# Kernel optimization log

Measured on AMD Instinct MI355X. Metric: run time of the kernel, lower is better.

## Reference

```python
import jax, jax.numpy as jnp
from jax import lax
import numpy as np


def setup_inputs() -> dict:
    key = jax.random.key(0)
    ks = jax.random.split(key, 5)
    B = 256
    data = jax.random.normal(ks[0], (B, 1, 28, 28), jnp.float32)
    # ConvLayer: Conv2d(1->256, k=9, s=1)
    w1 = jax.random.normal(ks[1], (256, 1, 9, 9), jnp.float32) * 0.1
    b1 = jnp.zeros((256,), jnp.float32)
    # PrimaryCaps: Conv2d(256->256, k=9, s=2)
    w2 = jax.random.normal(ks[2], (256, 256, 9, 9), jnp.float32) * 0.02
    b2 = jnp.zeros((256,), jnp.float32)
    # DigitCaps routing weights: (in_caps=1152, out_caps=10, out_len=16, in_len=8)
    W = jax.random.normal(ks[3], (1152, 10, 16, 8), jnp.float32) * 0.05
    return {"data": data, "w1": w1, "b1": b1, "w2": w2, "b2": b2, "W": W}


def _squash(s):
    # s: (B,1,10,16); sn*s / ((1+sn)*sqrt(sn)) as in the torch code
    sn = jnp.sum(s * s, axis=-1, keepdims=True)
    return sn * s / ((1.0 + sn) * jnp.sqrt(sn))


def reference(data, w1, b1, w2, b2, W):
    # ConvLayer: conv k9 s1 VALID + relu -> (B,256,20,20)
    x = lax.conv(data, w1, (1, 1), 'VALID') + b1[None, :, None, None]
    x = jax.nn.relu(x)
    # PrimaryCaps: conv k9 s2 VALID -> (B,256,6,6)
    x = lax.conv(x, w2, (2, 2), 'VALID') + b2[None, :, None, None]
    B = x.shape[0]
    # toCapsules: (B,256,6,6) -> (B,8,32,6,6) -> (B,8,1152) -> (B,1152,8)
    x = x.reshape(B, 8, -1).transpose(0, 2, 1)
    # u_hat[b,n,o,k] = W[n,o,k,d] @ x[b,n,d]  -> (B,1152,10,16)
    u_hat = jnp.einsum('nokd,bnd->bnok', W, x)
    b_ij = jnp.zeros((B, 1152, 10, 1), u_hat.dtype)
    num_iterations = 3
    v_j = None
    for it in range(1, num_iterations + 1):
        c_ij = jax.nn.softmax(b_ij, axis=1)            # over input capsules
        s_j = jnp.sum(c_ij * u_hat, axis=1, keepdims=True)  # (B,1,10,16)
        v_j = _squash(s_j)
        if it < num_iterations:
            # Faithful to the torch code: a_ij = u_hat * sum_k(v_j), broadcast
            # over input capsules; b_ij widens to (B,1152,10,16) after iter 1.
            a_ij = u_hat * jnp.sum(v_j, axis=-1, keepdims=True)
            b_ij = b_ij + a_ij
    return v_j[:, 0]  # (B,10,16)
```

## Files before the change

kernel.cpp:

```cpp
#include <hip/hip_runtime.h>
#include <hip/hip_bf16.h>
#include <cmath>


typedef float f32x4 __attribute__((ext_vector_type(4)));
typedef short s16x8 __attribute__((ext_vector_type(8)));
typedef unsigned int u32;

static __device__ __forceinline__ short f2bf(float x) {
  __hip_bfloat16 h = __float2bfloat16(x);
  return *reinterpret_cast<short*>(&h);
}
static __device__ __forceinline__ float bf2f(short s) {
  __hip_bfloat16 h;
  *reinterpret_cast<short*>(&h) = s;
  return __bfloat162float(h);
}
static __device__ __forceinline__ void stage16(const short* g, short* l) {
  __builtin_amdgcn_global_load_lds(
      (const __attribute__((address_space(1))) u32*)(const void*)g,
      (__attribute__((address_space(3))) u32*)(void*)l, 16, 0, 0);
}

#define CHUNK_SHORTS 23552
#define ODD_OFS 12288

__global__ __launch_bounds__(256) void prep_all(
    const float* __restrict__ w2, s16x8* __restrict__ wstg,
    const float* __restrict__ data, const float* __restrict__ w1,
    const float* __restrict__ b1, short* __restrict__ c1g) {
  __shared__ float sbuf[12784];
  const int t = threadIdx.x;
  if (blockIdx.x < 512) {
    const int b = blockIdx.x;
    const int chunk = b >> 6;
    const int kg = (b >> 4) & 3;
    const int cot = b & 15;
    const int co0 = cot * 16;
    const size_t gbase = (size_t)(chunk * 32 + kg * 8) * 81;
    for (int i = t; i < 10368; i += 256) {
      const int r = i / 648, e = i - r * 648;
      sbuf[i] = w2[(size_t)(co0 + r) * 20736 + gbase + e];
    }
    __syncthreads();
    for (int p = t; p < 1296; p += 256) {
      const int tap = p >> 4, co = p & 15;
      s16x8 hi, lo;
#pragma unroll
      for (int i = 0; i < 8; ++i) {
        const float x = sbuf[co * 648 + i * 81 + tap];
        const short h = f2bf(x);
        hi[i] = h;
        lo[i] = f2bf(x - bf2f(h));
      }
      const size_t T = (size_t)(chunk * 81 + tap);
      wstg[T * 2048 + kg * 256 + co0 + co] = hi;
      wstg[T * 2048 + 1024 + kg * 256 + co0 + co] = lo;
    }
    return;
  }
  const int cb = blockIdx.x - 512;
  const int img = cb >> 1;
  const int chh = cb & 1;
  float* simg = sbuf;
  short* c1buf = (short*)&sbuf[1008];
  for (int i = t; i < 784; i += 256)
    simg[(i / 28) * 36 + (i % 28)] = data[img * 784 + i];
  __syncthreads();
  for (int cc = 0; cc < 4; ++cc) {
    const int chunk = chh * 4 + cc;
    for (int task = t; task < 608; task += 256) {
      const int ci = task & 31;
      const int y = task >> 5;
      const int ch = chunk * 32 + ci;
      const float* wr = w1 + ch * 81;
      float acc[20];
      const float bz = b1[ch];
#pragma unroll
      for (int x = 0; x < 20; ++x) acc[x] = bz;
#pragma unroll
      for (int ky = 0; ky < 9; ++ky) {
        float rr[28];
#pragma unroll
        for (int q = 0; q < 7; ++q)
          *(float4*)&rr[q * 4] = *(const float4*)&simg[(y + ky) * 36 + q * 4];
#pragma unroll
        for (int kx = 0; kx < 9; ++kx) {
          const float w = wr[ky * 9 + kx];
#pragma unroll
          for (int x = 0; x < 20; ++x) acc[x] = fmaf(w, rr[x + kx], acc[x]);
        }
      }
      const int kg = ci >> 3, il = ci & 7;
#pragma unroll
      for (int x = 0; x < 19; ++x) {
        const int xh = x >> 1;
        const int r = (x & 1) ? (y * 9 + xh) : (y * 10 + xh);
        short* base = c1buf + ((x & 1) ? ODD_OFS : 0);
        const float v = fmaxf(acc[x], 0.f);
        const short hi = f2bf(v);
        const short lo = f2bf(v - bf2f(hi));
        base[r * 64 + (((kg + r) & 7) << 3) + il] = hi;
        base[r * 64 + (((kg + 4 + r) & 7) << 3) + il] = lo;
      }
    }
    __syncthreads();
    {
      s16x8* dst = (s16x8*)(c1g + (size_t)(img * 8 + chunk) * CHUNK_SHORTS);
      const s16x8* srcb = (const s16x8*)c1buf;
      for (int i = t; i < 2944; i += 256) dst[i] = srcb[i];
    }
    __syncthreads();
  }
}

__global__ __launch_bounds__(256) void conv2_mfma(
    const short* __restrict__ c1g, const short* __restrict__ wstg,
    const float* __restrict__ b2, float* __restrict__ xcaps0,
    float* __restrict__ xcaps1) {
  const int t = threadIdx.x;
  const int bid = blockIdx.x;
  const int xcd = bid & 7;
  const int ksp = xcd & 1;
  const int coh = (xcd >> 1) & 1;
  const int img = (bid >> 3) * 2 + (xcd >> 2);
  const int lane = t & 63;
  const int wv = t >> 6;
  const int r16 = lane & 15;
  const int kg = lane >> 4;

  __shared__ short c1[12288];

  int arowE[3], arowO[3];
#pragma unroll
  for (int m = 0; m < 3; ++m) {
    int pos = m * 16 + r16;
    if (pos > 35) pos = 35;
    const int oy = pos / 6, ox = pos % 6;
    arowE[m] = oy * 20 + ox;
    arowO[m] = oy * 18 + ox;
  }
  int bOff[2], con[2];
  float bias[2];
#pragma unroll
  for (int j = 0; j < 2; ++j) {
    const int co = coh * 128 + wv * 32 + j * 16 + r16;
    con[j] = co;
    bOff[j] = kg * 256 + co;
    bias[j] = (ksp == 0) ? b2[co] : 0.f;
  }
  float* xcp = (ksp == 0) ? xcaps0 : xcaps1;

  const f32x4 vzero = {0.f, 0.f, 0.f, 0.f};
  f32x4 acc[3][2];
#pragma unroll
  for (int m = 0; m < 3; ++m)
#pragma unroll
    for (int j = 0; j < 2; ++j) acc[m][j] = vzero;

  const s16x8* wsv = (const s16x8*)wstg;

  for (int cc = 0; cc < 4; ++cc) {
    const int chunk = ksp * 4 + cc;
    const short* src = c1g + (size_t)(img * 8 + chunk) * CHUNK_SHORTS;
    const size_t bb = (size_t)chunk * 81 * 2048;

    __syncthreads();
    for (int c = wv; c < 24; c += 4)
      stage16(src + c * 512 + lane * 8, &c1[c * 512]);
    __syncthreads();
    {
      s16x8 BHc[2], BLc[2];
#pragma unroll
      for (int j = 0; j < 2; ++j) {
        BHc[j] = wsv[bb + bOff[j]];
        BLc[j] = wsv[bb + bOff[j] + 1024];
      }
      for (int ky = 0; ky < 9; ++ky) {
#pragma unroll
        for (int kxi = 0; kxi < 5; ++kxi) {
          s16x8 BHn[2], BLn[2];
          if (!(ky == 8 && kxi == 4)) {
            const int nky = (kxi == 4) ? ky + 1 : ky;
            const int nkxi = (kxi == 4) ? 0 : kxi + 1;
            const size_t nb = bb + (size_t)(nky * 9 + 2 * nkxi) * 2048;
#pragma unroll
            for (int j = 0; j < 2; ++j) {
              BHn[j] = wsv[nb + bOff[j]];
              BLn[j] = wsv[nb + bOff[j] + 1024];
            }
          }
          s16x8 AH[3], AL[3];
#pragma unroll
          for (int m = 0; m < 3; ++m) {
            const int r = arowE[m] + ky * 10 + kxi;
            AH[m] = *(const s16x8*)&c1[r * 64 + (((kg + r) & 7) << 3)];
            AL[m] = *(const s16x8*)&c1[r * 64 + (((kg + 4 + r) & 7) << 3)];
          }
          __builtin_amdgcn_s_setprio(1);
#pragma unroll
          for (int m = 0; m < 3; ++m)
#pragma unroll
            for (int j = 0; j < 2; ++j)
              acc[m][j] = __builtin_amdgcn_mfma_f32_16x16x32_bf16(AH[m], BHc[j], acc[m][j], 0, 0, 0);
#pragma unroll
          for (int m = 0; m < 3; ++m)
#pragma unroll
            for (int j = 0; j < 2; ++j)
              acc[m][j] = __builtin_amdgcn_mfma_f32_16x16x32_bf16(AL[m], BHc[j], acc[m][j], 0, 0, 0);
#pragma unroll
          for (int m = 0; m < 3; ++m)
#pragma unroll
            for (int j = 0; j < 2; ++j)
              acc[m][j] = __builtin_amdgcn_mfma_f32_16x16x32_bf16(AH[m], BLc[j], acc[m][j], 0, 0, 0);
          __builtin_amdgcn_s_setprio(0);
#pragma unroll
          for (int j = 0; j < 2; ++j) { BHc[j] = BHn[j]; BLc[j] = BLn[j]; }
        }
      }
    }

    __syncthreads();
    for (int c = wv; c < 22; c += 4)
      stage16(src + ODD_OFS + c * 512 + lane * 8, &c1[c * 512]);
    __syncthreads();
    {
      s16x8 BHc[2], BLc[2];
#pragma unroll
      for (int j = 0; j < 2; ++j) {
        BHc[j] = wsv[bb + 2048 + bOff[j]];
        BLc[j] = wsv[bb + 2048 + bOff[j] + 1024];
      }
      for (int ky = 0; ky < 9; ++ky) {
#pragma unroll
        for (int kxi = 0; kxi < 4; ++kxi) {
          s16x8 BHn[2], BLn[2];
          if (!(ky == 8 && kxi == 3)) {
            const int nky = (kxi == 3) ? ky + 1 : ky;
            const int nkxi = (kxi == 3) ? 0 : kxi + 1;
            const size_t nb = bb + (size_t)(nky * 9 + 2 * nkxi + 1) * 2048;
#pragma unroll
            for (int j = 0; j < 2; ++j) {
              BHn[j] = wsv[nb + bOff[j]];
              BLn[j] = wsv[nb + bOff[j] + 1024];
            }
          }
          s16x8 AH[3], AL[3];
#pragma unroll
          for (int m = 0; m < 3; ++m) {
            const int r = arowO[m] + ky * 9 + kxi;
            AH[m] = *(const s16x8*)&c1[r * 64 + (((kg + r) & 7) << 3)];
            AL[m] = *(const s16x8*)&c1[r * 64 + (((kg + 4 + r) & 7) << 3)];
          }
          __builtin_amdgcn_s_setprio(1);
#pragma unroll
          for (int m = 0; m < 3; ++m)
#pragma unroll
            for (int j = 0; j < 2; ++j)
              acc[m][j] = __builtin_amdgcn_mfma_f32_16x16x32_bf16(AH[m], BHc[j], acc[m][j], 0, 0, 0);
#pragma unroll
          for (int m = 0; m < 3; ++m)
#pragma unroll
            for (int j = 0; j < 2; ++j)
              acc[m][j] = __builtin_amdgcn_mfma_f32_16x16x32_bf16(AL[m], BHc[j], acc[m][j], 0, 0, 0);
#pragma unroll
          for (int m = 0; m < 3; ++m)
#pragma unroll
            for (int j = 0; j < 2; ++j)
              acc[m][j] = __builtin_amdgcn_mfma_f32_16x16x32_bf16(AH[m], BLc[j], acc[m][j], 0, 0, 0);
          __builtin_amdgcn_s_setprio(0);
#pragma unroll
          for (int j = 0; j < 2; ++j) { BHc[j] = BHn[j]; BLc[j] = BLn[j]; }
        }
      }
    }
  }

#pragma unroll
  for (int m = 0; m < 3; ++m) {
#pragma unroll
    for (int jj = 0; jj < 4; ++jj) {
      const int pos = m * 16 + kg * 4 + jj;
      if (pos < 36) {
#pragma unroll
        for (int j = 0; j < 2; ++j) {
          const int co = con[j];
          const int n = (co & 31) * 36 + pos;
          xcp[((size_t)img * 1152 + n) * 8 + (co >> 5)] = acc[m][j][jj] + bias[j];
        }
      }
    }
  }
}

__global__ __launch_bounds__(256) void routing_fused(const float* __restrict__ xcaps0,
                                                     const float* __restrict__ xcaps1,
                                                     const float* __restrict__ W,
                                                     float* __restrict__ out) {
  const int o = blockIdx.x >> 7;
  const int bp = blockIdx.x & 127;
  const int b0 = bp * 2, b1 = b0 + 1;
  const int t = threadIdx.x;
  const int k = t & 15, ng = t >> 4;
  __shared__ float xs0[1152 * 8];
  __shared__ float xs1[1152 * 8];
  __shared__ double redA[256], redB[256], redC[256], redD[256];
  __shared__ float s0s[16], s1s[16];
  __shared__ float sv0, sv1;
  __shared__ double f0, f1;

  {
    const float4* p00 = (const float4*)(xcaps0 + (size_t)b0 * 9216);
    const float4* p01 = (const float4*)(xcaps1 + (size_t)b0 * 9216);
    const float4* p10 = (const float4*)(xcaps0 + (size_t)b1 * 9216);
    const float4* p11 = (const float4*)(xcaps1 + (size_t)b1 * 9216);
    float4* d0 = (float4*)xs0;
    float4* d1 = (float4*)xs1;
    for (int i = t; i < 2304; i += 256) {
      float4 a = p00[i], b = p01[i];
      float4 c = p10[i], d = p11[i];
      float4 s0, s1;
      s0.x = a.x + b.x; s0.y = a.y + b.y; s0.z = a.z + b.z; s0.w = a.w + b.w;
      s1.x = c.x + d.x; s1.y = c.y + d.y; s1.z = c.z + d.z; s1.w = c.w + d.w;
      d0[i] = s0;
      d1[i] = s1;
    }
  }
  __syncthreads();

  const int n0 = ng * 72;
  float u0[72], u1[72];
  const float* wp = W + ((size_t)(n0 * 10 + o) * 16 + k) * 8;
#pragma unroll
  for (int i = 0; i < 72; ++i) {
    const float* wq = wp + (size_t)i * 1280;
    const float4 wa = *(const float4*)wq;
    const float4 wb = *(const float4*)(wq + 4);
    const float4 xa0 = *(const float4*)&xs0[(n0 + i) * 8];
    const float4 xb0 = *(const float4*)&xs0[(n0 + i) * 8 + 4];
    const float4 xa1 = *(const float4*)&xs1[(n0 + i) * 8];
    const float4 xb1 = *(const float4*)&xs1[(n0 + i) * 8 + 4];
    float s0 = wa.x * xa0.x + wa.y * xa0.y + wa.z * xa0.z + wa.w * xa0.w
             + wb.x * xb0.x + wb.y * xb0.y + wb.z * xb0.z + wb.w * xb0.w;
    float s1 = wa.x * xa1.x + wa.y * xa1.y + wa.z * xa1.z + wa.w * xa1.w
             + wb.x * xb1.x + wb.y * xb1.y + wb.z * xb1.z + wb.w * xb1.w;
    u0[i] = s0;
    u1[i] = s1;
  }

  {
    double S0 = 0.0, S1 = 0.0;
#pragma unroll
    for (int i = 0; i < 72; ++i) { S0 += (double)u0[i]; S1 += (double)u1[i]; }
    redA[t] = S0; redB[t] = S1;
  }
  __syncthreads();
  if (t < 16) {
    double t0 = 0.0, t1 = 0.0;
#pragma unroll
    for (int g = 0; g < 16; ++g) { t0 += redA[g * 16 + t]; t1 += redB[g * 16 + t]; }
    s0s[t] = (float)(t0 * (double)(1.0f / 1152.0f));
    s1s[t] = (float)(t1 * (double)(1.0f / 1152.0f));
  }
  __syncthreads();
  if (t == 0) {
    double sn = 0.0;
#pragma unroll
    for (int kk = 0; kk < 16; ++kk) sn += (double)s0s[kk] * (double)s0s[kk];
    double f = sn / ((1.0 + sn) * sqrt(sn));
    double sv = 0.0;
#pragma unroll
    for (int kk = 0; kk < 16; ++kk) sv += (double)s0s[kk] * f;
    sv0 = (float)sv;
    sn = 0.0;
#pragma unroll
    for (int kk = 0; kk < 16; ++kk) sn += (double)s1s[kk] * (double)s1s[kk];
    f = sn / ((1.0 + sn) * sqrt(sn));
    sv = 0.0;
#pragma unroll
    for (int kk = 0; kk < 16; ++kk) sv += (double)s1s[kk] * f;
    sv1 = (float)sv;
  }
  __syncthreads();
  const float v10 = sv0, v11 = sv1;

  {
    double E0 = 0.0, EU0 = 0.0, E1 = 0.0, EU1 = 0.0;
#pragma unroll
    for (int i = 0; i < 72; ++i) {
      const float e0 = expf(u0[i] * v10);
      E0 += (double)e0;
      EU0 += (double)e0 * (double)u0[i];
      const float e1 = expf(u1[i] * v11);
      E1 += (double)e1;
      EU1 += (double)e1 * (double)u1[i];
    }
    redA[t] = E0; redB[t] = EU0; redC[t] = E1; redD[t] = EU1;
  }
  __syncthreads();
  if (t < 16) {
    double e0 = 0.0, s0 = 0.0, e1 = 0.0, s1 = 0.0;
#pragma unroll
    for (int g = 0; g < 16; ++g) {
      e0 += redA[g * 16 + t]; s0 += redB[g * 16 + t];
      e1 += redC[g * 16 + t]; s1 += redD[g * 16 + t];
    }
    s0s[t] = (float)(s0 / e0);
    s1s[t] = (float)(s1 / e1);
  }
  __syncthreads();
  if (t == 0) {
    double sn = 0.0;
#pragma unroll
    for (int kk = 0; kk < 16; ++kk) sn += (double)s0s[kk] * (double)s0s[kk];
    double f = sn / ((1.0 + sn) * sqrt(sn));
    double sv = 0.0;
#pragma unroll
    for (int kk = 0; kk < 16; ++kk) sv += (double)s0s[kk] * f;
    sv0 = v10 + (float)sv;
    sn = 0.0;
#pragma unroll
    for (int kk = 0; kk < 16; ++kk) sn += (double)s1s[kk] * (double)s1s[kk];
    f = sn / ((1.0 + sn) * sqrt(sn));
    sv = 0.0;
#pragma unroll
    for (int kk = 0; kk < 16; ++kk) sv += (double)s1s[kk] * f;
    sv1 = v11 + (float)sv;
  }
  __syncthreads();
  const float v20 = sv0, v21 = sv1;

  {
    double E0 = 0.0, EU0 = 0.0, E1 = 0.0, EU1 = 0.0;
#pragma unroll
    for (int i = 0; i < 72; ++i) {
      const float e0 = expf(u0[i] * v20);
      E0 += (double)e0;
      EU0 += (double)e0 * (double)u0[i];
      const float e1 = expf(u1[i] * v21);
      E1 += (double)e1;
      EU1 += (double)e1 * (double)u1[i];
    }
    redA[t] = E0; redB[t] = EU0; redC[t] = E1; redD[t] = EU1;
  }
  __syncthreads();
  if (t < 16) {
    double e0 = 0.0, s0 = 0.0, e1 = 0.0, s1 = 0.0;
#pragma unroll
    for (int g = 0; g < 16; ++g) {
      e0 += redA[g * 16 + t]; s0 += redB[g * 16 + t];
      e1 += redC[g * 16 + t]; s1 += redD[g * 16 + t];
    }
    s0s[t] = (float)(s0 / e0);
    s1s[t] = (float)(s1 / e1);
  }
  __syncthreads();
  if (t == 0) {
    double sn = 0.0;
#pragma unroll
    for (int kk = 0; kk < 16; ++kk) sn += (double)s0s[kk] * (double)s0s[kk];
    f0 = sn / ((1.0 + sn) * sqrt(sn));
    sn = 0.0;
#pragma unroll
    for (int kk = 0; kk < 16; ++kk) sn += (double)s1s[kk] * (double)s1s[kk];
    f1 = sn / ((1.0 + sn) * sqrt(sn));
  }
  __syncthreads();
  if (t < 16) {
    out[b0 * 160 + o * 16 + t] = (float)((double)s0s[t] * f0);
    out[b1 * 160 + o * 16 + t] = (float)((double)s1s[t] * f1);
  }
}

extern "C" void kernel_launch(void* const* d_in, const int* in_sizes, int n_in,
                              void* d_out, int out_size, void* d_ws, size_t ws_size,
                              hipStream_t stream) {
  const float* data = (const float*)d_in[0];
  const float* w1   = (const float*)d_in[1];
  const float* b1   = (const float*)d_in[2];
  const float* w2   = (const float*)d_in[3];
  const float* b2   = (const float*)d_in[4];
  const float* W    = (const float*)d_in[5];
  float* out = (float*)d_out;

  short* wstg   = (short*)d_ws;
  short* c1g    = wstg + 10616832;
  float* xcaps0 = (float*)(c1g + 48234496);
  float* xcaps1 = xcaps0 + 2359296;

  prep_all<<<1024, 256, 0, stream>>>(w2, (s16x8*)wstg, data, w1, b1, c1g);
  conv2_mfma<<<1024, 256, 0, stream>>>(c1g, wstg, b2, xcaps0, xcaps1);
  routing_fused<<<1280, 256, 0, stream>>>(xcaps0, xcaps1, W, out);
}
```

Baseline: 507.1 us.

## Process two images per conv2 block to reuse weight fragments across more rows

Each conv2 block now stacks two images into the M dimension, giving 5 row tiles (72 positions) instead of 3 (36 padded to 48). The conv1 activations for both images are staged into a doubled LDS buffer, and the grid is halved to 512 blocks. This amortizes the global weight-fragment loads over more MFMAs and cuts padding waste, at the cost of more accumulator registers, twice the LDS per block, and fewer blocks for occupancy.

After: 465.2 us. 8.3% less time.

```diff
diff --git a/kernel.cpp b/kernel.cpp
--- a/kernel.cpp
+++ b/kernel.cpp
@@ -24,6 +24,8 @@
 
 #define CHUNK_SHORTS 23552
 #define ODD_OFS 12288
+#define EV_IMG 12288
+#define OD_IMG 11264
 
 __global__ __launch_bounds__(256) void prep_all(
     const float* __restrict__ w2, s16x8* __restrict__ wstg,
@@ -123,22 +125,27 @@
   const int xcd = bid & 7;
   const int ksp = xcd & 1;
   const int coh = (xcd >> 1) & 1;
-  const int img = (bid >> 3) * 2 + (xcd >> 2);
+  const int pair = (bid >> 3) * 2 + (xcd >> 2);
+  const int img0 = pair * 2;
   const int lane = t & 63;
   const int wv = t >> 6;
   const int r16 = lane & 15;
   const int kg = lane >> 4;
 
-  __shared__ short c1[12288];
-
-  int arowE[3], arowO[3];
-#pragma unroll
-  for (int m = 0; m < 3; ++m) {
-    int pos = m * 16 + r16;
-    if (pos > 35) pos = 35;
-    const int oy = pos / 6, ox = pos % 6;
+  __shared__ short c1[24576];
+
+  int arowE[5], arowO[5], imE[5], imO[5];
+#pragma unroll
+  for (int m = 0; m < 5; ++m) {
+    const int s = m * 16 + r16;
+    const int im = (s >= 36) ? 1 : 0;
+    int p = s - 36 * im;
+    if (p > 35) p = 35;
+    const int oy = p / 6, ox = p % 6;
     arowE[m] = oy * 20 + ox;
     arowO[m] = oy * 18 + ox;
+    imE[m] = im * EV_IMG;
+    imO[m] = im * OD_IMG;
   }
   int bOff[2], con[2];
   float bias[2];
@@ -152,9 +159,9 @@
   float* xcp = (ksp == 0) ? xcaps0 : xcaps1;
 
   const f32x4 vzero = {0.f, 0.f, 0.f, 0.f};
-  f32x4 acc[3][2];
-#pragma unroll
-  for (int m = 0; m < 3; ++m)
+  f32x4 acc[5][2];
+#pragma unroll
+  for (int m = 0; m < 5; ++m)
 #pragma unroll
     for (int j = 0; j < 2; ++j) acc[m][j] = vzero;
 
@@ -162,12 +169,15 @@
 
   for (int cc = 0; cc < 4; ++cc) {
     const int chunk = ksp * 4 + cc;
-    const short* src = c1g + (size_t)(img * 8 + chunk) * CHUNK_SHORTS;
+    const short* src0 = c1g + (size_t)(img0 * 8 + chunk) * CHUNK_SHORTS;
+    const short* src1 = c1g + (size_t)((img0 + 1) * 8 + chunk) * CHUNK_SHORTS;
     const size_t bb = (size_t)chunk * 81 * 2048;
 
     __syncthreads();
-    for (int c = wv; c < 24; c += 4)
-      stage16(src + c * 512 + lane * 8, &c1[c * 512]);
+    for (int c = wv; c < 48; c += 4) {
+      const short* s = (c < 24) ? (src0 + c * 512) : (src1 + (c - 24) * 512);
+      stage16(s + lane * 8, &c1[c * 512]);
+    }
     __syncthreads();
     {
       s16x8 BHc[2], BLc[2];
@@ -190,26 +200,26 @@
               BLn[j] = wsv[nb + bOff[j] + 1024];
             }
           }
-          s16x8 AH[3], AL[3];
-#pragma unroll
-          for (int m = 0; m < 3; ++m) {
+          s16x8 AH[5], AL[5];
+#pragma unroll
+          for (int m = 0; m < 5; ++m) {
             const int r = arowE[m] + ky * 10 + kxi;
-            AH[m] = *(const s16x8*)&c1[r * 64 + (((kg + r) & 7) << 3)];
-            AL[m] = *(const s16x8*)&c1[r * 64 + (((kg + 4 + r) & 7) << 3)];
+            AH[m] = *(const s16x8*)&c1[imE[m] + r * 64 + (((kg + r) & 7) << 3)];
+            AL[m] = *(const s16x8*)&c1[imE[m] + r * 64 + (((kg + 4 + r) & 7) << 3)];
           }
           __builtin_amdgcn_s_setprio(1);
 #pragma unroll
-          for (int m = 0; m < 3; ++m)
+          for (int m = 0; m < 5; ++m)
 #pragma unroll
             for (int j = 0; j < 2; ++j)
               acc[m][j] = __builtin_amdgcn_mfma_f32_16x16x32_bf16(AH[m], BHc[j], acc[m][j], 0, 0, 0);
 #pragma unroll
-          for (int m = 0; m < 3; ++m)
+          for (int m = 0; m < 5; ++m)
 #pragma unroll
             for (int j = 0; j < 2; ++j)
               acc[m][j] = __builtin_amdgcn_mfma_f32_16x16x32_bf16(AL[m], BHc[j], acc[m][j], 0, 0, 0);
 #pragma unroll
-          for (int m = 0; m < 3; ++m)
+          for (int m = 0; m < 5; ++m)
 #pragma unroll
             for (int j = 0; j < 2; ++j)
               acc[m][j] = __builtin_amdgcn_mfma_f32_16x16x32_bf16(AH[m], BLc[j], acc[m][j], 0, 0, 0);
@@ -221,8 +231,11 @@
     }
 
     __syncthreads();
-    for (int c = wv; c < 22; c += 4)
-      stage16(src + ODD_OFS + c * 512 + lane * 8, &c1[c * 512]);
+    for (int c = wv; c < 44; c += 4) {
+      const short* s = (c < 22) ? (src0 + ODD_OFS + c * 512)
+                                : (src1 + ODD_OFS + (c - 22) * 512);
+      stage16(s + lane * 8, &c1[c * 512]);
+    }
     __syncthreads();
     {
       s16x8 BHc[2], BLc[2];
@@ -245,26 +258,26 @@
               BLn[j] = wsv[nb + bOff[j] + 1024];
             }
           }
-          s16x8 AH[3], AL[3];
-#pragma unroll
-          for (int m = 0; m < 3; ++m) {
+          s16x8 AH[5], AL[5];
+#pragma unroll
+          for (int m = 0; m < 5; ++m) {
             const int r = arowO[m] + ky * 9 + kxi;
-            AH[m] = *(const s16x8*)&c1[r * 64 + (((kg + r) & 7) << 3)];
-            AL[m] = *(const s16x8*)&c1[r * 64 + (((kg + 4 + r) & 7) << 3)];
+            AH[m] = *(const s16x8*)&c1[imO[m] + r * 64 + (((kg + r) & 7) << 3)];
+            AL[m] = *(const s16x8*)&c1[imO[m] + r * 64 + (((kg + 4 + r) & 7) << 3)];
           }
           __builtin_amdgcn_s_setprio(1);
 #pragma unroll
-          for (int m = 0; m < 3; ++m)
+          for (int m = 0; m < 5; ++m)
 #pragma unroll
             for (int j = 0; j < 2; ++j)
               acc[m][j] = __builtin_amdgcn_mfma_f32_16x16x32_bf16(AH[m], BHc[j], acc[m][j], 0, 0, 0);
 #pragma unroll
-          for (int m = 0; m < 3; ++m)
+          for (int m = 0; m < 5; ++m)
 #pragma unroll
             for (int j = 0; j < 2; ++j)
               acc[m][j] = __builtin_amdgcn_mfma_f32_16x16x32_bf16(AL[m], BHc[j], acc[m][j], 0, 0, 0);
 #pragma unroll
-          for (int m = 0; m < 3; ++m)
+          for (int m = 0; m < 5; ++m)
 #pragma unroll
             for (int j = 0; j < 2; ++j)
               acc[m][j] = __builtin_amdgcn_mfma_f32_16x16x32_bf16(AH[m], BLc[j], acc[m][j], 0, 0, 0);
@@ -277,16 +290,19 @@
   }
 
 #pragma unroll
-  for (int m = 0; m < 3; ++m) {
+  for (int m = 0; m < 5; ++m) {
 #pragma unroll
     for (int jj = 0; jj < 4; ++jj) {
-      const int pos = m * 16 + kg * 4 + jj;
-      if (pos < 36) {
+      const int s = m * 16 + kg * 4 + jj;
+      if (s < 72) {
+        const int im = (s >= 36) ? 1 : 0;
+        const int p = s - 36 * im;
 #pragma unroll
         for (int j = 0; j < 2; ++j) {
           const int co = con[j];
-          const int n = (co & 31) * 36 + pos;
-          xcp[((size_t)img * 1152 + n) * 8 + (co >> 5)] = acc[m][j][jj] + bias[j];
+          const int n = (co & 31) * 36 + p;
+          xcp[((size_t)(img0 + im) * 1152 + n) * 8 + (co >> 5)] =
+              acc[m][j][jj] + bias[j];
         }
       }
     }
@@ -489,6 +505,6 @@
   float* xcaps1 = xcaps0 + 2359296;
 
   prep_all<<<1024, 256, 0, stream>>>(w2, (s16x8*)wstg, data, w1, b1, c1g);
-  conv2_mfma<<<1024, 256, 0, stream>>>(c1g, wstg, b2, xcaps0, xcaps1);
+  conv2_mfma<<<512, 256, 0, stream>>>(c1g, wstg, b2, xcaps0, xcaps1);
   routing_fused<<<1280, 256, 0, stream>>>(xcaps0, xcaps1, W, out);
 }
```
